# Optimization experiments

Measured on AMD Instinct MI355X. Metric: run time of the kernel, lower is better.

## Reference

```python
import jax, jax.numpy as jnp
import numpy as np

NEG_INF = -1e30  # stands in for -math.inf in masked_fill; -inf itself also works in fp32


def setup_inputs() -> dict:
    key = jax.random.key(0)
    k1, k2, k3, k4, k5 = jax.random.split(key, 5)
    B, T, S, H = 32, 512, 1024, 1024
    query = jax.random.normal(k1, (B, T, H), dtype=jnp.float32)
    encoder_outputs = jax.random.normal(k2, (S, B, H), dtype=jnp.float32)  # seq-first, as in torch RNN outputs
    src_lengths = jax.random.randint(k3, (B,), 1, S + 1, dtype=jnp.int32)
    W_in = jax.random.normal(k4, (H, H), dtype=jnp.float32) / np.sqrt(H)
    W_out = jax.random.normal(k5, (H, 2 * H), dtype=jnp.float32) / np.sqrt(2 * H)
    b_out = jnp.zeros((H,), dtype=jnp.float32)
    return {"query": query, "encoder_outputs": encoder_outputs, "src_lengths": src_lengths,
            "W_in": W_in, "W_out": W_out, "b_out": b_out}


def reference(query, encoder_outputs, src_lengths, W_in, W_out, b_out):
    # query: [B,T,H]; encoder_outputs: [S,B,H] (seq-first)
    # NOTE: the original module computes a length mask but never applies it;
    # instead it fills positions where the raw score is exactly 0 with -inf.
    z = jnp.einsum('bth,ih->bti', query, W_in)                 # linear_in (no bias)
    scores = jnp.einsum('bti,sbi->bts', z, encoder_outputs)    # bmm -> [B,T,S]
    scores = jnp.where(scores == 0, jnp.float32(-jnp.inf), scores)
    p = jax.nn.softmax(scores, axis=2)                         # [B,T,S]
    c = jnp.einsum('bts,sbh->bth', p, encoder_outputs)         # context [B,T,H]
    cat = jnp.concatenate([c, query], axis=2)                  # [B,T,2H]
    attn_h_t = jnp.tanh(jnp.einsum('btk,hk->bth', cat, W_out) + b_out)
    return attn_h_t
```

## Files before the change

kernel.cpp:

```cpp
#include <hip/hip_runtime.h>
#include <math.h>


__device__ inline unsigned short f2bf(float x) {
    unsigned int u = __float_as_uint(x);
    u += 0x7fffu + ((u >> 16) & 1u);
    return (unsigned short)(u >> 16);
}
__device__ inline float bf2f(unsigned short h) {
    return __uint_as_float(((unsigned int)h) << 16);
}
__device__ inline unsigned short f2h(float x) {
    _Float16 h = (_Float16)x;
    return *(unsigned short*)&h;
}

typedef __attribute__((ext_vector_type(8))) short    short8;
typedef __attribute__((ext_vector_type(8))) _Float16 half8;
typedef __attribute__((ext_vector_type(4))) float    f32x4;

__device__ inline void gld_lds16(const void* g, void* l) {
    __builtin_amdgcn_global_load_lds(
        (const __attribute__((address_space(1))) unsigned int*)g,
        (__attribute__((address_space(3))) unsigned int*)l, 16, 0, 0);
}

__device__ inline short8 frag_ld(const short* Ls, int rowbase, int ks8, int lane) {
    const int r = lane & 15, q = lane >> 4;
    return *(const short8*)&Ls[(rowbase + r) * 64 + (((ks8 + q) ^ (r & 7)) << 3)];
}
__device__ inline half8 frag_ld_h(const short* Ls, int rowbase, int ks8, int lane) {
    const int r = lane & 15, q = lane >> 4;
    return *(const half8*)&Ls[(rowbase + r) * 64 + (((ks8 + q) ^ (r & 7)) << 3)];
}

__device__ inline void stage_tile(const unsigned short* g, long ld, short* lds,
                                  int rw, int lr, int gran) {
#pragma unroll
    for (int seg = 0; seg < 4; ++seg) {
        const int row = rw + seg * 8 + lr;
        gld_lds16(g + (long)row * ld + (gran << 3), lds + (rw + seg * 8) * 64);
    }
}

template<int OUT_MODE>
__global__ __launch_bounds__(256, 2)
void gemm_x3(const unsigned short* __restrict__ Ahg, const unsigned short* __restrict__ Alg,
             const unsigned short* __restrict__ Bhg, const unsigned short* __restrict__ Blg,
             float* __restrict__ Of, unsigned short* __restrict__ Oh,
             unsigned short* __restrict__ Ol,
             int K, long lda, long ldb, long ldc, long sA, long sB, long sC)
{
    __shared__ short Ah[128 * 64], Al[128 * 64], Bh[128 * 64], Bl[128 * 64];

    const int tid  = threadIdx.x;
    const int wave = tid >> 6, lane = tid & 63;
    const int wm = (wave & 1) << 6, wn = (wave >> 1) << 6;
    const long m0 = (long)blockIdx.y * 128, n0 = (long)blockIdx.x * 128;
    const int bz = blockIdx.z;

    const unsigned short* Ah0 = Ahg + (long)bz * sA + m0 * lda;
    const unsigned short* Al0 = Alg + (long)bz * sA + m0 * lda;
    const unsigned short* Bh0 = Bhg + (long)bz * sB + n0 * ldb;
    const unsigned short* Bl0 = Blg + (long)bz * sB + n0 * ldb;

    f32x4 acc[4][4];
#pragma unroll
    for (int i = 0; i < 4; ++i)
#pragma unroll
        for (int j = 0; j < 4; ++j) acc[i][j] = (f32x4){0.f, 0.f, 0.f, 0.f};

    const int lr   = lane >> 3;
    const int gran = (lane & 7) ^ lr;
    const int rw   = wave * 32;

    for (int k0 = 0; k0 < K; k0 += 64) {
        __syncthreads();
        stage_tile(Ah0 + k0, lda, Ah, rw, lr, gran);
        stage_tile(Al0 + k0, lda, Al, rw, lr, gran);
        stage_tile(Bh0 + k0, ldb, Bh, rw, lr, gran);
        stage_tile(Bl0 + k0, ldb, Bl, rw, lr, gran);
        __syncthreads();
#pragma unroll
        for (int ks = 0; ks < 2; ++ks) {
            short8 ah[4], al[4], bh[4], bl[4];
#pragma unroll
            for (int i = 0; i < 4; ++i) ah[i] = frag_ld(Ah, wm + i * 16, ks * 4, lane);
#pragma unroll
            for (int j = 0; j < 4; ++j) bh[j] = frag_ld(Bh, wn + j * 16, ks * 4, lane);
#pragma unroll
            for (int i = 0; i < 4; ++i)
#pragma unroll
                for (int j = 0; j < 4; ++j)
                    acc[i][j] = __builtin_amdgcn_mfma_f32_16x16x32_bf16(ah[i], bh[j], acc[i][j], 0, 0, 0);
#pragma unroll
            for (int j = 0; j < 4; ++j) bl[j] = frag_ld(Bl, wn + j * 16, ks * 4, lane);
#pragma unroll
            for (int i = 0; i < 4; ++i)
#pragma unroll
                for (int j = 0; j < 4; ++j)
                    acc[i][j] = __builtin_amdgcn_mfma_f32_16x16x32_bf16(ah[i], bl[j], acc[i][j], 0, 0, 0);
#pragma unroll
            for (int i = 0; i < 4; ++i) al[i] = frag_ld(Al, wm + i * 16, ks * 4, lane);
#pragma unroll
            for (int i = 0; i < 4; ++i)
#pragma unroll
                for (int j = 0; j < 4; ++j)
                    acc[i][j] = __builtin_amdgcn_mfma_f32_16x16x32_bf16(al[i], bh[j], acc[i][j], 0, 0, 0);
        }
    }

    const int q = lane >> 4, r = lane & 15;
#pragma unroll
    for (int i = 0; i < 4; ++i)
#pragma unroll
        for (int rr = 0; rr < 4; ++rr) {
            const long grow = m0 + wm + i * 16 + q * 4 + rr;
#pragma unroll
            for (int j = 0; j < 4; ++j) {
                const long gcol = n0 + wn + j * 16 + r;
                const float v = acc[i][j][rr];
                const long off = (long)bz * sC + grow * ldc + gcol;
                if constexpr (OUT_MODE == 1) {
                    unsigned short h = f2bf(v);
                    Oh[off] = h;
                    Ol[off] = f2bf(v - bf2f(h));
                } else {
                    Of[off] = v;
                }
            }
        }
}

template<int NCHUNK, int OUT_MODE>
__global__ __launch_bounds__(256, 2)
void gemm_f16(const unsigned short* __restrict__ A0, const unsigned short* __restrict__ A1,
              const unsigned short* __restrict__ B0, const unsigned short* __restrict__ B1,
              float* __restrict__ Of, unsigned short* __restrict__ Oh,
              const float* __restrict__ bias,
              int chunkK, long lda, long ldb, long ldc, long sA, long sB, long sC)
{
    __shared__ short As[128 * 64];
    __shared__ short Bs[128 * 64];

    const int tid  = threadIdx.x;
    const int wave = tid >> 6, lane = tid & 63;
    const int wm = (wave & 1) << 6, wn = (wave >> 1) << 6;
    const long m0 = (long)blockIdx.y * 128, n0 = (long)blockIdx.x * 128;
    const int bz = blockIdx.z;

    const unsigned short* Ap[2] = {A0, A1};
    const unsigned short* Bp[2] = {B0, B1};

    f32x4 acc[4][4];
#pragma unroll
    for (int i = 0; i < 4; ++i)
#pragma unroll
        for (int j = 0; j < 4; ++j) acc[i][j] = (f32x4){0.f, 0.f, 0.f, 0.f};

    const int lr   = lane >> 3;
    const int gran = (lane & 7) ^ lr;
    const int rw   = wave * 32;

#pragma unroll
    for (int c = 0; c < NCHUNK; ++c) {
        const unsigned short* Ac = Ap[c] + (long)bz * sA + m0 * lda;
        const unsigned short* Bc = Bp[c] + (long)bz * sB + n0 * ldb;
        for (int k0 = 0; k0 < chunkK; k0 += 64) {
            __syncthreads();
            stage_tile(Ac + k0, lda, As, rw, lr, gran);
            stage_tile(Bc + k0, ldb, Bs, rw, lr, gran);
            __syncthreads();
#pragma unroll
            for (int ks = 0; ks < 2; ++ks) {
                half8 af[4], bfv[4];
#pragma unroll
                for (int i = 0; i < 4; ++i) af[i]  = frag_ld_h(As, wm + i * 16, ks * 4, lane);
#pragma unroll
                for (int j = 0; j < 4; ++j) bfv[j] = frag_ld_h(Bs, wn + j * 16, ks * 4, lane);
#pragma unroll
                for (int i = 0; i < 4; ++i)
#pragma unroll
                    for (int j = 0; j < 4; ++j)
                        acc[i][j] = __builtin_amdgcn_mfma_f32_16x16x32_f16(af[i], bfv[j], acc[i][j], 0, 0, 0);
            }
        }
    }

    const int q = lane >> 4, r = lane & 15;
#pragma unroll
    for (int i = 0; i < 4; ++i)
#pragma unroll
        for (int rr = 0; rr < 4; ++rr) {
            const long grow = m0 + wm + i * 16 + q * 4 + rr;
#pragma unroll
            for (int j = 0; j < 4; ++j) {
                const long gcol = n0 + wn + j * 16 + r;
                const float v = acc[i][j][rr];
                const long off = (long)bz * sC + grow * ldc + gcol;
                if constexpr (OUT_MODE == 0) {
                    Oh[off] = f2h(v);
                } else {
                    Of[off] = tanhf(v + bias[gcol]);
                }
            }
        }
}

template<bool HAS_LO>
__global__ __launch_bounds__(256)
void split_f32_bf16(const float* __restrict__ x, unsigned short* __restrict__ hi,
                    unsigned short* __restrict__ lo, int n4)
{
    const int i = blockIdx.x * 256 + threadIdx.x;
    if (i >= n4) return;
    const float4 v = ((const float4*)x)[i];
    ushort4 h;
    h.x = f2bf(v.x); h.y = f2bf(v.y); h.z = f2bf(v.z); h.w = f2bf(v.w);
    ((ushort4*)hi)[i] = h;
    if constexpr (HAS_LO) {
        ushort4 l;
        l.x = f2bf(v.x - bf2f(h.x)); l.y = f2bf(v.y - bf2f(h.y));
        l.z = f2bf(v.z - bf2f(h.z)); l.w = f2bf(v.w - bf2f(h.w));
        ((ushort4*)lo)[i] = l;
    }
}

__global__ __launch_bounds__(256)
void conv_f32_f16(const float* __restrict__ x, unsigned short* __restrict__ o, int n4)
{
    const int i = blockIdx.x * 256 + threadIdx.x;
    if (i >= n4) return;
    const float4 v = ((const float4*)x)[i];
    ushort4 h;
    h.x = f2h(v.x); h.y = f2h(v.y); h.z = f2h(v.z); h.w = f2h(v.w);
    ((ushort4*)o)[i] = h;
}

__global__ __launch_bounds__(256)
void transpose_enc_f16(const float* __restrict__ E, unsigned short* __restrict__ ET)
{
    __shared__ unsigned short L[64][72];
    const int s0 = blockIdx.x * 64, h0 = blockIdx.y * 64, b = blockIdx.z;
    const int tid = threadIdx.x;
#pragma unroll
    for (int io = 0; io < 2; ++io) {
        const int g = io * 256 + tid;
        const int rs = g >> 3, c8 = (g & 7) * 8;
        const float* src = E + ((long)(s0 + rs) * 32 + b) * 1024 + h0 + c8;
        const float4 v0 = *(const float4*)(src);
        const float4 v1 = *(const float4*)(src + 4);
        L[rs][c8 + 0] = f2h(v0.x); L[rs][c8 + 1] = f2h(v0.y);
        L[rs][c8 + 2] = f2h(v0.z); L[rs][c8 + 3] = f2h(v0.w);
        L[rs][c8 + 4] = f2h(v1.x); L[rs][c8 + 5] = f2h(v1.y);
        L[rs][c8 + 6] = f2h(v1.z); L[rs][c8 + 7] = f2h(v1.w);
    }
    __syncthreads();
#pragma unroll
    for (int io = 0; io < 2; ++io) {
        const int g = io * 256 + tid;
        const int rh = g >> 3, c8 = (g & 7) * 8;
        unsigned short t[8];
#pragma unroll
        for (int j = 0; j < 8; ++j) t[j] = L[c8 + j][rh];
        unsigned short* dst = ET + ((long)b * 1024 + h0 + rh) * 1024 + s0 + c8;
        *(ushort4*)(dst)     = *(const ushort4*)&t[0];
        *(ushort4*)(dst + 4) = *(const ushort4*)&t[4];
    }
}

__global__ __launch_bounds__(256)
void softmax_p_f16(const float* __restrict__ P, unsigned short* __restrict__ Pb)
{
    const int row  = blockIdx.x * 4 + (threadIdx.x >> 6);
    const int lane = threadIdx.x & 63;
    const float* p = P + (long)row * 1024 + lane * 4;
    unsigned short* pb = Pb + (long)row * 1024 + lane * 4;

    float4 v[4];
    float mx = -INFINITY;
#pragma unroll
    for (int i = 0; i < 4; ++i) {
        v[i] = *(const float4*)(p + i * 256);
        v[i].x = (v[i].x == 0.f) ? -INFINITY : v[i].x;
        v[i].y = (v[i].y == 0.f) ? -INFINITY : v[i].y;
        v[i].z = (v[i].z == 0.f) ? -INFINITY : v[i].z;
        v[i].w = (v[i].w == 0.f) ? -INFINITY : v[i].w;
        mx = fmaxf(mx, fmaxf(fmaxf(v[i].x, v[i].y), fmaxf(v[i].z, v[i].w)));
    }
#pragma unroll
    for (int o = 32; o > 0; o >>= 1) mx = fmaxf(mx, __shfl_xor(mx, o, 64));

    float sum = 0.f;
#pragma unroll
    for (int i = 0; i < 4; ++i) {
        v[i].x = __expf(v[i].x - mx); v[i].y = __expf(v[i].y - mx);
        v[i].z = __expf(v[i].z - mx); v[i].w = __expf(v[i].w - mx);
        sum += v[i].x + v[i].y + v[i].z + v[i].w;
    }
#pragma unroll
    for (int o = 32; o > 0; o >>= 1) sum += __shfl_xor(sum, o, 64);

    const float inv = 1.f / sum;
#pragma unroll
    for (int i = 0; i < 4; ++i) {
        ushort4 u;
        u.x = f2h(v[i].x * inv); u.y = f2h(v[i].y * inv);
        u.z = f2h(v[i].z * inv); u.w = f2h(v[i].w * inv);
        *(ushort4*)(pb + i * 256) = u;
    }
}

#define BM 128
#define BN 128
#define BKT 16

template<bool BT, bool DO_TANH, bool CAT_A>
__global__ __launch_bounds__(256)
void sgemm(const float* __restrict__ A, const float* __restrict__ A2,
           const float* __restrict__ Bmat, const float* __restrict__ bias,
           float* __restrict__ C,
           int M, int N, int K, int Ksplit,
           int lda, int ldb, int ldc,
           long sA, long sB, long sC)
{
    __shared__ float Asb[BKT][BM];
    __shared__ float Bsb[BKT][BN];

    const int bz = blockIdx.z;
    const float* Ab = A + (long)bz * sA;
    const float* Bb = Bmat + (long)bz * sB;
    float* Cb = C + (long)bz * sC;

    const int tid = threadIdx.x;
    const int m0 = blockIdx.y * BM;
    const int n0 = blockIdx.x * BN;
    const int tx = tid & 15;
    const int ty = tid >> 4;

    float acc[8][8];
#pragma unroll
    for (int i = 0; i < 8; ++i)
#pragma unroll
        for (int j = 0; j < 8; ++j) acc[i][j] = 0.f;

    for (int kk = 0; kk < K; kk += BKT) {
        const float* Asrc = Ab;
        int acol = kk;
        if constexpr (CAT_A) {
            if (kk >= Ksplit) { Asrc = A2; acol = kk - Ksplit; }
        }
#pragma unroll
        for (int i = 0; i < 2; ++i) {
            int f = i * 256 + tid;
            int row = f >> 2;
            int k4 = (f & 3) << 2;
            float4 v = *(const float4*)(Asrc + (long)(m0 + row) * lda + acol + k4);
            Asb[k4 + 0][row] = v.x; Asb[k4 + 1][row] = v.y;
            Asb[k4 + 2][row] = v.z; Asb[k4 + 3][row] = v.w;
        }
        if constexpr (BT) {
#pragma unroll
            for (int i = 0; i < 2; ++i) {
                int f = i * 256 + tid;
                int row = f >> 2;
                int k4 = (f & 3) << 2;
                float4 v = *(const float4*)(Bb + (long)(n0 + row) * ldb + kk + k4);
                Bsb[k4 + 0][row] = v.x; Bsb[k4 + 1][row] = v.y;
                Bsb[k4 + 2][row] = v.z; Bsb[k4 + 3][row] = v.w;
            }
        } else {
#pragma unroll
            for (int i = 0; i < 2; ++i) {
                int f = i * 256 + tid;
                int kr = f >> 5;
                int n4 = (f & 31) << 2;
                float4 v = *(const float4*)(Bb + (long)(kk + kr) * ldb + n0 + n4);
                *(float4*)&Bsb[kr][n4] = v;
            }
        }
        __syncthreads();
#pragma unroll
        for (int k = 0; k < BKT; ++k) {
            float a[8], bv[8];
            *(float4*)&a[0]  = *(const float4*)&Asb[k][ty * 4];
            *(float4*)&a[4]  = *(const float4*)&Asb[k][ty * 4 + 64];
            *(float4*)&bv[0] = *(const float4*)&Bsb[k][tx * 4];
            *(float4*)&bv[4] = *(const float4*)&Bsb[k][tx * 4 + 64];
#pragma unroll
            for (int i = 0; i < 8; ++i)
#pragma unroll
                for (int j = 0; j < 8; ++j)
                    acc[i][j] = fmaf(a[i], bv[j], acc[i][j]);
        }
        __syncthreads();
    }
#pragma unroll
    for (int i = 0; i < 8; ++i) {
        int rrow = m0 + ty * 4 + (i & 3) + ((i >> 2) << 6);
        float* crow = Cb + (long)rrow * ldc;
#pragma unroll
        for (int jj = 0; jj < 2; ++jj) {
            int c0 = n0 + tx * 4 + jj * 64;
            float4 v;
            v.x = acc[i][jj * 4 + 0]; v.y = acc[i][jj * 4 + 1];
            v.z = acc[i][jj * 4 + 2]; v.w = acc[i][jj * 4 + 3];
            if constexpr (DO_TANH) {
                v.x = tanhf(v.x + bias[c0 + 0]); v.y = tanhf(v.y + bias[c0 + 1]);
                v.z = tanhf(v.z + bias[c0 + 2]); v.w = tanhf(v.w + bias[c0 + 3]);
            }
            *(float4*)(crow + c0) = v;
        }
    }
}

__global__ __launch_bounds__(256)
void softmax_rows(float* __restrict__ P)
{
    const int row = blockIdx.x * 4 + (threadIdx.x >> 6);
    const int lane = threadIdx.x & 63;
    float* p = P + (long)row * 1024 + lane * 4;
    float4 v[4];
    float mx = -INFINITY;
#pragma unroll
    for (int i = 0; i < 4; ++i) {
        v[i] = *(const float4*)(p + i * 256);
        v[i].x = (v[i].x == 0.f) ? -INFINITY : v[i].x;
        v[i].y = (v[i].y == 0.f) ? -INFINITY : v[i].y;
        v[i].z = (v[i].z == 0.f) ? -INFINITY : v[i].z;
        v[i].w = (v[i].w == 0.f) ? -INFINITY : v[i].w;
        mx = fmaxf(mx, fmaxf(fmaxf(v[i].x, v[i].y), fmaxf(v[i].z, v[i].w)));
    }
#pragma unroll
    for (int o = 32; o > 0; o >>= 1) mx = fmaxf(mx, __shfl_xor(mx, o, 64));
    float sum = 0.f;
#pragma unroll
    for (int i = 0; i < 4; ++i) {
        v[i].x = __expf(v[i].x - mx); v[i].y = __expf(v[i].y - mx);
        v[i].z = __expf(v[i].z - mx); v[i].w = __expf(v[i].w - mx);
        sum += v[i].x + v[i].y + v[i].z + v[i].w;
    }
#pragma unroll
    for (int o = 32; o > 0; o >>= 1) sum += __shfl_xor(sum, o, 64);
    const float inv = 1.f / sum;
#pragma unroll
    for (int i = 0; i < 4; ++i) {
        v[i].x *= inv; v[i].y *= inv; v[i].z *= inv; v[i].w *= inv;
        *(float4*)(p + i * 256) = v[i];
    }
}

extern "C" void kernel_launch(void* const* d_in, const int* in_sizes, int n_in,
                              void* d_out, int out_size, void* d_ws, size_t ws_size,
                              hipStream_t stream)
{
    (void)in_sizes; (void)n_in; (void)out_size;
    const int Bv = 32, T = 512, S = 1024, H = 1024;

    const float* q     = (const float*)d_in[0];
    const float* enc   = (const float*)d_in[1];
    const float* W_in  = (const float*)d_in[3];
    const float* W_out = (const float*)d_in[4];
    const float* b_out = (const float*)d_in[5];
    float* out = (float*)d_out;

    const size_t need = 264ull << 20;
    if (ws_size >= need) {
        char* w = (char*)d_ws;
        unsigned short* q_hi  = (unsigned short*)(w);
        unsigned short* q_lo  = (unsigned short*)(w + (32ull << 20));
        unsigned short* z_hi  = (unsigned short*)(w + (64ull << 20));
        unsigned short* z_lo  = (unsigned short*)(w + (96ull << 20));
        unsigned short* e_hi  = (unsigned short*)(w + (128ull << 20));
        unsigned short* e_lo  = (unsigned short*)(w + (192ull << 20));
        unsigned short* Wi_hi = (unsigned short*)(w + (256ull << 20));
        unsigned short* Wi_lo = (unsigned short*)(w + (258ull << 20));
        unsigned short* Wo16  = (unsigned short*)(w + (260ull << 20));

        unsigned short* Pb    = q_lo;
        unsigned short* q16   = z_lo;
        unsigned short* eT    = e_lo;
        unsigned short* C16   = z_hi;

        split_f32_bf16<true ><<<16384, 256, 0, stream>>>(q, q_hi, q_lo, 4194304);
        split_f32_bf16<true ><<<1024,  256, 0, stream>>>(W_in, Wi_hi, Wi_lo, 262144);
        conv_f32_f16<<<2048, 256, 0, stream>>>(W_out, Wo16, 524288);
        split_f32_bf16<true ><<<32768, 256, 0, stream>>>(enc, e_hi, e_lo, 8388608);

        gemm_x3<1><<<dim3(8, 128, 1), 256, 0, stream>>>(
            q_hi, q_lo, Wi_hi, Wi_lo,
            nullptr, z_hi, z_lo,
            1024, 1024, 1024, 1024, 0, 0, 0);

        gemm_x3<2><<<dim3(8, 4, 32), 256, 0, stream>>>(
            z_hi, z_lo, e_hi, e_lo,
            (float*)d_out, nullptr, nullptr,
            1024, 1024, (long)Bv * H, 1024,
            (long)T * H, (long)H, (long)T * S);

        softmax_p_f16<<<(Bv * T) / 4, 256, 0, stream>>>((const float*)d_out, Pb);

        conv_f32_f16<<<16384, 256, 0, stream>>>(q, q16, 4194304);

        transpose_enc_f16<<<dim3(16, 16, 32), 256, 0, stream>>>(enc, eT);

        gemm_f16<1, 0><<<dim3(8, 4, 32), 256, 0, stream>>>(
            Pb, nullptr, eT, nullptr,
            nullptr, C16, nullptr,
            1024, 1024, 1024, 1024,
            (long)T * S, (long)H * S, (long)T * H);

        gemm_f16<2, 3><<<dim3(8, 128, 1), 256, 0, stream>>>(
            C16, q16, Wo16, Wo16 + 1024,
            (float*)d_out, nullptr, b_out,
            1024, 1024, 2048, 1024, 0, 0, 0);
    } else {
        float* Z = (float*)d_ws;
        float* P = Z + (size_t)Bv * T * H;
        dim3 blk(256);
        sgemm<true, false, false><<<dim3(H / BN, (Bv * T) / BM, 1), blk, 0, stream>>>(
            q, nullptr, W_in, nullptr, Z,
            Bv * T, H, H, 0, H, H, H, 0, 0, 0);
        sgemm<true, false, false><<<dim3(S / BN, T / BM, Bv), blk, 0, stream>>>(
            Z, nullptr, enc, nullptr, P,
            T, S, H, 0, H, Bv * H, S, (long)T * H, H, (long)T * S);
        softmax_rows<<<(Bv * T) / 4, blk, 0, stream>>>(P);
        sgemm<false, false, false><<<dim3(H / BN, T / BM, Bv), blk, 0, stream>>>(
            P, nullptr, enc, nullptr, Z,
            T, H, S, 0, S, Bv * H, H, (long)T * S, H, (long)T * H);
        sgemm<true, true, true><<<dim3(H / BN, (Bv * T) / BM, 1), blk, 0, stream>>>(
            Z, q, W_out, b_out, out,
            Bv * T, H, 2 * H, H, H, 2 * H, H, 0, 0, 0);
    }
}
```

Before: 727.4 us.

## Unify GEMMs into triple-buffered 256x128 prefetch-pipelined MFMA kernel

Replaces the separate split-bf16 GEMM and f16 GEMM kernels with one templated kernel, gemm8p. It uses 512 threads and 256x128 tiles. Operands stream through a three-slot LDS ring via global_load_lds, prefetched two K-steps ahead with partial vmcnt waits, so global loads overlap MFMA work. The three-product split-precision sum is rewritten as a 3-chunk concatenated K loop, and MFMA phases are wrapped in s_setprio. The larger tile and ring buffer raise LDS use to about 147KB, which limits occupancy to one block per CU.

```diff
diff --git a/kernel.cpp b/kernel.cpp
--- a/kernel.cpp
+++ b/kernel.cpp
@@ -25,97 +25,155 @@
         (__attribute__((address_space(3))) unsigned int*)l, 16, 0, 0);
 }
 
+#define BAR() do { asm volatile("" ::: "memory"); \
+                   __builtin_amdgcn_s_barrier();  \
+                   asm volatile("" ::: "memory"); } while (0)
+#define VM6() asm volatile("s_waitcnt vmcnt(6)" ::: "memory")
+#define VM0() asm volatile("s_waitcnt vmcnt(0)" ::: "memory")
+
 __device__ inline short8 frag_ld(const short* Ls, int rowbase, int ks8, int lane) {
     const int r = lane & 15, q = lane >> 4;
     return *(const short8*)&Ls[(rowbase + r) * 64 + (((ks8 + q) ^ (r & 7)) << 3)];
 }
-__device__ inline half8 frag_ld_h(const short* Ls, int rowbase, int ks8, int lane) {
-    const int r = lane & 15, q = lane >> 4;
-    return *(const half8*)&Ls[(rowbase + r) * 64 + (((ks8 + q) ^ (r & 7)) << 3)];
-}
-
-__device__ inline void stage_tile(const unsigned short* g, long ld, short* lds,
-                                  int rw, int lr, int gran) {
-#pragma unroll
-    for (int seg = 0; seg < 4; ++seg) {
-        const int row = rw + seg * 8 + lr;
-        gld_lds16(g + (long)row * ld + (gran << 3), lds + (rw + seg * 8) * 64);
-    }
-}
-
-template<int OUT_MODE>
-__global__ __launch_bounds__(256, 2)
-void gemm_x3(const unsigned short* __restrict__ Ahg, const unsigned short* __restrict__ Alg,
-             const unsigned short* __restrict__ Bhg, const unsigned short* __restrict__ Blg,
-             float* __restrict__ Of, unsigned short* __restrict__ Oh,
-             unsigned short* __restrict__ Ol,
-             int K, long lda, long ldb, long ldc, long sA, long sB, long sC)
-{
-    __shared__ short Ah[128 * 64], Al[128 * 64], Bh[128 * 64], Bl[128 * 64];
+
+template<int DT>
+__device__ inline f32x4 mfma16(short8 a, short8 b, f32x4 c) {
+    if constexpr (DT == 0)
+        return __builtin_amdgcn_mfma_f32_16x16x32_bf16(a, b, c, 0, 0, 0);
+    else
+        return __builtin_amdgcn_mfma_f32_16x16x32_f16(
+            __builtin_bit_cast(half8, a), __builtin_bit_cast(half8, b), c, 0, 0, 0);
+}
+
+__device__ inline void stage1(const unsigned short* gk, long ld, short* slot,
+                              int rowbase , int lane) {
+    const int row = rowbase + (lane >> 3);
+    const int g   = (lane & 7) ^ (row & 7);
+    gld_lds16(gk + (long)row * ld + (g << 3), slot + rowbase * 64);
+}
+
+template<int DT, int OUT_MODE>
+__global__ __launch_bounds__(512, 2)
+void gemm8p(const unsigned short* __restrict__ A0, const unsigned short* __restrict__ A1,
+            const unsigned short* __restrict__ A2,
+            const unsigned short* __restrict__ B0, const unsigned short* __restrict__ B1,
+            const unsigned short* __restrict__ B2,
+            float* __restrict__ Of, unsigned short* __restrict__ Oh,
+            unsigned short* __restrict__ Ol, const float* __restrict__ bias,
+            int NT, long lda, long ldb, long ldc, long sA, long sB, long sC)
+{
+    __shared__ short LA[3 * 256 * 64];
+    __shared__ short LB[3 * 128 * 64];
 
     const int tid  = threadIdx.x;
-    const int wave = tid >> 6, lane = tid & 63;
-    const int wm = (wave & 1) << 6, wn = (wave >> 1) << 6;
-    const long m0 = (long)blockIdx.y * 128, n0 = (long)blockIdx.x * 128;
+    const int wid  = tid >> 6, lane = tid & 63;
+    const int wm   = (wid & 3) << 6;
+    const int wn   = (wid >> 2) << 6;
+    const int rb8  = wid << 3;
+    const long m0 = (long)blockIdx.y * 256, n0 = (long)blockIdx.x * 128;
     const int bz = blockIdx.z;
 
-    const unsigned short* Ah0 = Ahg + (long)bz * sA + m0 * lda;
-    const unsigned short* Al0 = Alg + (long)bz * sA + m0 * lda;
-    const unsigned short* Bh0 = Bhg + (long)bz * sB + n0 * ldb;
-    const unsigned short* Bl0 = Blg + (long)bz * sB + n0 * ldb;
-
     f32x4 acc[4][4];
 #pragma unroll
     for (int i = 0; i < 4; ++i)
 #pragma unroll
         for (int j = 0; j < 4; ++j) acc[i][j] = (f32x4){0.f, 0.f, 0.f, 0.f};
 
-    const int lr   = lane >> 3;
-    const int gran = (lane & 7) ^ lr;
-    const int rw   = wave * 32;
-
-    for (int k0 = 0; k0 < K; k0 += 64) {
-        __syncthreads();
-        stage_tile(Ah0 + k0, lda, Ah, rw, lr, gran);
-        stage_tile(Al0 + k0, lda, Al, rw, lr, gran);
-        stage_tile(Bh0 + k0, ldb, Bh, rw, lr, gran);
-        stage_tile(Bl0 + k0, ldb, Bl, rw, lr, gran);
-        __syncthreads();
-#pragma unroll
-        for (int ks = 0; ks < 2; ++ks) {
-            short8 ah[4], al[4], bh[4], bl[4];
-#pragma unroll
-            for (int i = 0; i < 4; ++i) ah[i] = frag_ld(Ah, wm + i * 16, ks * 4, lane);
-#pragma unroll
-            for (int j = 0; j < 4; ++j) bh[j] = frag_ld(Bh, wn + j * 16, ks * 4, lane);
+    {
+        const unsigned short* Ab = A0 + (long)bz * sA + m0 * lda;
+        const unsigned short* Bb = B0 + (long)bz * sB + n0 * ldb;
+#pragma unroll
+        for (int pt = 0; pt < 2; ++pt) {
+            const unsigned short* Ag = Ab + pt * 64;
+            const unsigned short* Bg = Bb + pt * 64;
+            short* As = LA + pt * 16384;
+            short* Bs = LB + pt * 8192;
+            stage1(Ag, lda, As, 0   + rb8, lane);
+            stage1(Ag, lda, As, 64  + rb8, lane);
+            stage1(Ag, lda, As, 128 + rb8, lane);
+            stage1(Ag, lda, As, 192 + rb8, lane);
+            stage1(Bg, ldb, Bs, 0   + rb8, lane);
+            stage1(Bg, ldb, Bs, 64  + rb8, lane);
+        }
+        VM6();
+        BAR();
+    }
+
+    for (int t = 0; t < NT; ++t) {
+        const int s = t % 3;
+        const short* As = LA + s * 16384;
+        const short* Bs = LB + s * 8192;
+
+        const int t2 = t + 2;
+        const bool st = t2 < NT;
+        const unsigned short* A2g = nullptr;
+        const unsigned short* B2g = nullptr;
+        short* As2 = nullptr;
+        short* Bs2 = nullptr;
+        if (st) {
+            const int c2 = t2 >> 4;
+            const long kk2 = (long)(t2 & 15) << 6;
+            const unsigned short* Ac = (c2 == 0) ? A0 : ((c2 == 1) ? A1 : A2);
+            const unsigned short* Bc = (c2 == 0) ? B0 : ((c2 == 1) ? B1 : B2);
+            A2g = Ac + (long)bz * sA + m0 * lda + kk2;
+            B2g = Bc + (long)bz * sB + n0 * ldb + kk2;
+            const int s2 = t2 % 3;
+            As2 = LA + s2 * 16384;
+            Bs2 = LB + s2 * 8192;
+        }
+
+        {
+            short8 a[4], b[4];
+#pragma unroll
+            for (int i = 0; i < 4; ++i) a[i] = frag_ld(As, wm + i * 16, 0, lane);
+#pragma unroll
+            for (int j = 0; j < 4; ++j) b[j] = frag_ld(Bs, wn + j * 16, 0, lane);
+            if (st) {
+                stage1(A2g, lda, As2, 0   + rb8, lane);
+                stage1(A2g, lda, As2, 64  + rb8, lane);
+                stage1(A2g, lda, As2, 128 + rb8, lane);
+            }
+            BAR();
+            __builtin_amdgcn_s_setprio(1);
 #pragma unroll
             for (int i = 0; i < 4; ++i)
 #pragma unroll
                 for (int j = 0; j < 4; ++j)
-                    acc[i][j] = __builtin_amdgcn_mfma_f32_16x16x32_bf16(ah[i], bh[j], acc[i][j], 0, 0, 0);
-#pragma unroll
-            for (int j = 0; j < 4; ++j) bl[j] = frag_ld(Bl, wn + j * 16, ks * 4, lane);
+                    acc[i][j] = mfma16<DT>(a[i], b[j], acc[i][j]);
+            __builtin_amdgcn_s_setprio(0);
+            BAR();
+        }
+
+        {
+            short8 a[4], b[4];
+#pragma unroll
+            for (int i = 0; i < 4; ++i) a[i] = frag_ld(As, wm + i * 16, 4, lane);
+#pragma unroll
+            for (int j = 0; j < 4; ++j) b[j] = frag_ld(Bs, wn + j * 16, 4, lane);
+            if (st) {
+                stage1(A2g, lda, As2, 192 + rb8, lane);
+                stage1(B2g, ldb, Bs2, 0   + rb8, lane);
+                stage1(B2g, ldb, Bs2, 64  + rb8, lane);
+            }
+            if (st) VM6(); else VM0();
+            BAR();
+            __builtin_amdgcn_s_setprio(1);
 #pragma unroll
             for (int i = 0; i < 4; ++i)
 #pragma unroll
                 for (int j = 0; j < 4; ++j)
-                    acc[i][j] = __builtin_amdgcn_mfma_f32_16x16x32_bf16(ah[i], bl[j], acc[i][j], 0, 0, 0);
-#pragma unroll
-            for (int i = 0; i < 4; ++i) al[i] = frag_ld(Al, wm + i * 16, ks * 4, lane);
-#pragma unroll
-            for (int i = 0; i < 4; ++i)
-#pragma unroll
-                for (int j = 0; j < 4; ++j)
-                    acc[i][j] = __builtin_amdgcn_mfma_f32_16x16x32_bf16(al[i], bh[j], acc[i][j], 0, 0, 0);
-        }
-    }
-
-    const int q = lane >> 4, r = lane & 15;
+                    acc[i][j] = mfma16<DT>(a[i], b[j], acc[i][j]);
+            __builtin_amdgcn_s_setprio(0);
+            BAR();
+        }
+    }
+
+    const int qq = lane >> 4, r = lane & 15;
 #pragma unroll
     for (int i = 0; i < 4; ++i)
 #pragma unroll
         for (int rr = 0; rr < 4; ++rr) {
-            const long grow = m0 + wm + i * 16 + q * 4 + rr;
+            const long grow = m0 + wm + i * 16 + qq * 4 + rr;
 #pragma unroll
             for (int j = 0; j < 4; ++j) {
                 const long gcol = n0 + wn + j * 16 + r;
@@ -125,80 +183,9 @@
                     unsigned short h = f2bf(v);
                     Oh[off] = h;
                     Ol[off] = f2bf(v - bf2f(h));
-                } else {
+                } else if constexpr (OUT_MODE == 2) {
                     Of[off] = v;
-                }
-            }
-        }
-}
-
-template<int NCHUNK, int OUT_MODE>
-__global__ __launch_bounds__(256, 2)
-void gemm_f16(const unsigned short* __restrict__ A0, const unsigned short* __restrict__ A1,
-              const unsigned short* __restrict__ B0, const unsigned short* __restrict__ B1,
-              float* __restrict__ Of, unsigned short* __restrict__ Oh,
-              const float* __restrict__ bias,
-              int chunkK, long lda, long ldb, long ldc, long sA, long sB, long sC)
-{
-    __shared__ short As[128 * 64];
-    __shared__ short Bs[128 * 64];
-
-    const int tid  = threadIdx.x;
-    const int wave = tid >> 6, lane = tid & 63;
-    const int wm = (wave & 1) << 6, wn = (wave >> 1) << 6;
-    const long m0 = (long)blockIdx.y * 128, n0 = (long)blockIdx.x * 128;
-    const int bz = blockIdx.z;
-
-    const unsigned short* Ap[2] = {A0, A1};
-    const unsigned short* Bp[2] = {B0, B1};
-
-    f32x4 acc[4][4];
-#pragma unroll
-    for (int i = 0; i < 4; ++i)
-#pragma unroll
-        for (int j = 0; j < 4; ++j) acc[i][j] = (f32x4){0.f, 0.f, 0.f, 0.f};
-
-    const int lr   = lane >> 3;
-    const int gran = (lane & 7) ^ lr;
-    const int rw   = wave * 32;
-
-#pragma unroll
-    for (int c = 0; c < NCHUNK; ++c) {
-        const unsigned short* Ac = Ap[c] + (long)bz * sA + m0 * lda;
-        const unsigned short* Bc = Bp[c] + (long)bz * sB + n0 * ldb;
-        for (int k0 = 0; k0 < chunkK; k0 += 64) {
-            __syncthreads();
-            stage_tile(Ac + k0, lda, As, rw, lr, gran);
-            stage_tile(Bc + k0, ldb, Bs, rw, lr, gran);
-            __syncthreads();
-#pragma unroll
-            for (int ks = 0; ks < 2; ++ks) {
-                half8 af[4], bfv[4];
-#pragma unroll
-                for (int i = 0; i < 4; ++i) af[i]  = frag_ld_h(As, wm + i * 16, ks * 4, lane);
-#pragma unroll
-                for (int j = 0; j < 4; ++j) bfv[j] = frag_ld_h(Bs, wn + j * 16, ks * 4, lane);
-#pragma unroll
-                for (int i = 0; i < 4; ++i)
-#pragma unroll
-                    for (int j = 0; j < 4; ++j)
-                        acc[i][j] = __builtin_amdgcn_mfma_f32_16x16x32_f16(af[i], bfv[j], acc[i][j], 0, 0, 0);
-            }
-        }
-    }
-
-    const int q = lane >> 4, r = lane & 15;
-#pragma unroll
-    for (int i = 0; i < 4; ++i)
-#pragma unroll
-        for (int rr = 0; rr < 4; ++rr) {
-            const long grow = m0 + wm + i * 16 + q * 4 + rr;
-#pragma unroll
-            for (int j = 0; j < 4; ++j) {
-                const long gcol = n0 + wn + j * 16 + r;
-                const float v = acc[i][j][rr];
-                const long off = (long)bz * sC + grow * ldc + gcol;
-                if constexpr (OUT_MODE == 0) {
+                } else if constexpr (OUT_MODE == 0) {
                     Oh[off] = f2h(v);
                 } else {
                     Of[off] = tanhf(v + bias[gcol]);
@@ -487,16 +474,15 @@
         conv_f32_f16<<<2048, 256, 0, stream>>>(W_out, Wo16, 524288);
         split_f32_bf16<true ><<<32768, 256, 0, stream>>>(enc, e_hi, e_lo, 8388608);
 
-        gemm_x3<1><<<dim3(8, 128, 1), 256, 0, stream>>>(
-            q_hi, q_lo, Wi_hi, Wi_lo,
-            nullptr, z_hi, z_lo,
-            1024, 1024, 1024, 1024, 0, 0, 0);
-
-        gemm_x3<2><<<dim3(8, 4, 32), 256, 0, stream>>>(
-            z_hi, z_lo, e_hi, e_lo,
-            (float*)d_out, nullptr, nullptr,
-            1024, 1024, (long)Bv * H, 1024,
-            (long)T * H, (long)H, (long)T * S);
+        gemm8p<0, 1><<<dim3(8, 64, 1), 512, 0, stream>>>(
+            q_hi, q_lo, q_hi, Wi_hi, Wi_hi, Wi_lo,
+            nullptr, z_hi, z_lo, nullptr,
+            48, 1024, 1024, 1024, 0, 0, 0);
+
+        gemm8p<0, 2><<<dim3(8, 2, 32), 512, 0, stream>>>(
+            z_hi, z_lo, z_hi, e_hi, e_hi, e_lo,
+            (float*)d_out, nullptr, nullptr, nullptr,
+            48, 1024, (long)Bv * H, 1024, (long)T * H, (long)H, (long)T * S);
 
         softmax_p_f16<<<(Bv * T) / 4, 256, 0, stream>>>((const float*)d_out, Pb);
 
@@ -504,16 +490,15 @@
 
         transpose_enc_f16<<<dim3(16, 16, 32), 256, 0, stream>>>(enc, eT);
 
-        gemm_f16<1, 0><<<dim3(8, 4, 32), 256, 0, stream>>>(
-            Pb, nullptr, eT, nullptr,
-            nullptr, C16, nullptr,
-            1024, 1024, 1024, 1024,
-            (long)T * S, (long)H * S, (long)T * H);
-
-        gemm_f16<2, 3><<<dim3(8, 128, 1), 256, 0, stream>>>(
-            C16, q16, Wo16, Wo16 + 1024,
-            (float*)d_out, nullptr, b_out,
-            1024, 1024, 2048, 1024, 0, 0, 0);
+        gemm8p<1, 0><<<dim3(8, 2, 32), 512, 0, stream>>>(
+            Pb, nullptr, nullptr, eT, nullptr, nullptr,
+            nullptr, C16, nullptr, nullptr,
+            16, 1024, 1024, 1024, (long)T * S, (long)H * S, (long)T * H);
+
+        gemm8p<1, 3><<<dim3(8, 64, 1), 512, 0, stream>>>(
+            C16, q16, nullptr, Wo16, Wo16 + 1024, nullptr,
+            (float*)d_out, nullptr, nullptr, b_out,
+            32, 1024, 2048, 1024, 0, 0, 0);
     } else {
         float* Z = (float*)d_ws;
         float* P = Z + (size_t)Bv * T * H;
```

Measured after the change: 833.0 us. 14.5% more time.

## Fuse input conversion passes and add XCD-aware block swizzle for flat GEMMs

Applied to the files above, without the earlier changes.

When the workspace is large enough, the query split also writes the fp16 copy, and the encoder split also writes the fp16 transposed copy. This removes the separate re-reads of q and enc that happened later. The two weight-prep kernels are merged into one launch, and the two non-batched GEMMs remap block indices so that each XCD works on a contiguous range of tiles, which should improve L2 reuse. The fused path needs extra workspace (360MB), and if that is not available it falls back to the old aliased buffers.

```diff
diff --git a/kernel.cpp b/kernel.cpp
--- a/kernel.cpp
+++ b/kernel.cpp
@@ -43,7 +43,17 @@
     }
 }
 
-template<int OUT_MODE>
+__device__ inline void xcd_swz(int& bx, int& by) {
+    const int gx = gridDim.x;
+    const int nwg = gx * gridDim.y;
+    const int lin = by * gx + bx;
+    const int cpx = nwg >> 3;
+    const int swz = (lin & 7) * cpx + (lin >> 3);
+    bx = swz % gx;
+    by = swz / gx;
+}
+
+template<int OUT_MODE, bool SWZ>
 __global__ __launch_bounds__(256, 2)
 void gemm_x3(const unsigned short* __restrict__ Ahg, const unsigned short* __restrict__ Alg,
              const unsigned short* __restrict__ Bhg, const unsigned short* __restrict__ Blg,
@@ -56,7 +66,9 @@
     const int tid  = threadIdx.x;
     const int wave = tid >> 6, lane = tid & 63;
     const int wm = (wave & 1) << 6, wn = (wave >> 1) << 6;
-    const long m0 = (long)blockIdx.y * 128, n0 = (long)blockIdx.x * 128;
+    int bxi = blockIdx.x, byi = blockIdx.y;
+    if constexpr (SWZ) xcd_swz(bxi, byi);
+    const long m0 = (long)byi * 128, n0 = (long)bxi * 128;
     const int bz = blockIdx.z;
 
     const unsigned short* Ah0 = Ahg + (long)bz * sA + m0 * lda;
@@ -132,7 +144,7 @@
         }
 }
 
-template<int NCHUNK, int OUT_MODE>
+template<int NCHUNK, int OUT_MODE, bool SWZ>
 __global__ __launch_bounds__(256, 2)
 void gemm_f16(const unsigned short* __restrict__ A0, const unsigned short* __restrict__ A1,
               const unsigned short* __restrict__ B0, const unsigned short* __restrict__ B1,
@@ -146,7 +158,9 @@
     const int tid  = threadIdx.x;
     const int wave = tid >> 6, lane = tid & 63;
     const int wm = (wave & 1) << 6, wn = (wave >> 1) << 6;
-    const long m0 = (long)blockIdx.y * 128, n0 = (long)blockIdx.x * 128;
+    int bxi = blockIdx.x, byi = blockIdx.y;
+    if constexpr (SWZ) xcd_swz(bxi, byi);
+    const long m0 = (long)byi * 128, n0 = (long)bxi * 128;
     const int bz = blockIdx.z;
 
     const unsigned short* Ap[2] = {A0, A1};
@@ -207,23 +221,41 @@
         }
 }
 
-template<bool HAS_LO>
-__global__ __launch_bounds__(256)
-void split_f32_bf16(const float* __restrict__ x, unsigned short* __restrict__ hi,
-                    unsigned short* __restrict__ lo, int n4)
+template<bool Q16>
+__global__ __launch_bounds__(256)
+void split_q_k(const float* __restrict__ x, unsigned short* __restrict__ hi,
+               unsigned short* __restrict__ lo, unsigned short* __restrict__ h16,
+               int n4)
 {
     const int i = blockIdx.x * 256 + threadIdx.x;
     if (i >= n4) return;
     const float4 v = ((const float4*)x)[i];
-    ushort4 h;
+    ushort4 h, l;
     h.x = f2bf(v.x); h.y = f2bf(v.y); h.z = f2bf(v.z); h.w = f2bf(v.w);
+    l.x = f2bf(v.x - bf2f(h.x)); l.y = f2bf(v.y - bf2f(h.y));
+    l.z = f2bf(v.z - bf2f(h.z)); l.w = f2bf(v.w - bf2f(h.w));
     ((ushort4*)hi)[i] = h;
-    if constexpr (HAS_LO) {
-        ushort4 l;
-        l.x = f2bf(v.x - bf2f(h.x)); l.y = f2bf(v.y - bf2f(h.y));
-        l.z = f2bf(v.z - bf2f(h.z)); l.w = f2bf(v.w - bf2f(h.w));
-        ((ushort4*)lo)[i] = l;
-    }
+    ((ushort4*)lo)[i] = l;
+    if constexpr (Q16) {
+        ushort4 f;
+        f.x = f2h(v.x); f.y = f2h(v.y); f.z = f2h(v.z); f.w = f2h(v.w);
+        ((ushort4*)h16)[i] = f;
+    }
+}
+
+__global__ __launch_bounds__(256)
+void split_f32_bf16(const float* __restrict__ x, unsigned short* __restrict__ hi,
+                    unsigned short* __restrict__ lo, int n4)
+{
+    const int i = blockIdx.x * 256 + threadIdx.x;
+    if (i >= n4) return;
+    const float4 v = ((const float4*)x)[i];
+    ushort4 h, l;
+    h.x = f2bf(v.x); h.y = f2bf(v.y); h.z = f2bf(v.z); h.w = f2bf(v.w);
+    l.x = f2bf(v.x - bf2f(h.x)); l.y = f2bf(v.y - bf2f(h.y));
+    l.z = f2bf(v.z - bf2f(h.z)); l.w = f2bf(v.w - bf2f(h.w));
+    ((ushort4*)hi)[i] = h;
+    ((ushort4*)lo)[i] = l;
 }
 
 __global__ __launch_bounds__(256)
@@ -235,6 +267,72 @@
     ushort4 h;
     h.x = f2h(v.x); h.y = f2h(v.y); h.z = f2h(v.z); h.w = f2h(v.w);
     ((ushort4*)o)[i] = h;
+}
+
+__global__ __launch_bounds__(256)
+void prep_w_k(const float* __restrict__ Wi, unsigned short* __restrict__ Wih,
+              unsigned short* __restrict__ Wil,
+              const float* __restrict__ Wo, unsigned short* __restrict__ Wo16)
+{
+    const int i = blockIdx.x * 256 + threadIdx.x;
+    if (i < 262144) {
+        const float4 v = ((const float4*)Wi)[i];
+        ushort4 h, l;
+        h.x = f2bf(v.x); h.y = f2bf(v.y); h.z = f2bf(v.z); h.w = f2bf(v.w);
+        l.x = f2bf(v.x - bf2f(h.x)); l.y = f2bf(v.y - bf2f(h.y));
+        l.z = f2bf(v.z - bf2f(h.z)); l.w = f2bf(v.w - bf2f(h.w));
+        ((ushort4*)Wih)[i] = h;
+        ((ushort4*)Wil)[i] = l;
+    } else {
+        const int j = i - 262144;
+        if (j < 524288) {
+            const float4 v = ((const float4*)Wo)[j];
+            ushort4 h;
+            h.x = f2h(v.x); h.y = f2h(v.y); h.z = f2h(v.z); h.w = f2h(v.w);
+            ((ushort4*)Wo16)[j] = h;
+        }
+    }
+}
+
+__global__ __launch_bounds__(256)
+void split_enc_t(const float* __restrict__ E, unsigned short* __restrict__ Eh,
+                 unsigned short* __restrict__ El, unsigned short* __restrict__ ET)
+{
+    __shared__ unsigned short L[64][72];
+    const int s0 = blockIdx.x * 64, h0 = blockIdx.y * 64, b = blockIdx.z;
+    const int tid = threadIdx.x;
+#pragma unroll
+    for (int io = 0; io < 2; ++io) {
+        const int g = io * 256 + tid;
+        const int rs = g >> 3, c8 = (g & 7) * 8;
+        const long base = ((long)(s0 + rs) * 32 + b) * 1024 + h0 + c8;
+        const float4 v0 = *(const float4*)(E + base);
+        const float4 v1 = *(const float4*)(E + base + 4);
+        const float vv[8] = {v0.x, v0.y, v0.z, v0.w, v1.x, v1.y, v1.z, v1.w};
+        unsigned short hi[8], lo[8];
+#pragma unroll
+        for (int j = 0; j < 8; ++j) {
+            hi[j] = f2bf(vv[j]);
+            lo[j] = f2bf(vv[j] - bf2f(hi[j]));
+            L[rs][c8 + j] = f2h(vv[j]);
+        }
+        *(ushort4*)(Eh + base)     = *(const ushort4*)&hi[0];
+        *(ushort4*)(Eh + base + 4) = *(const ushort4*)&hi[4];
+        *(ushort4*)(El + base)     = *(const ushort4*)&lo[0];
+        *(ushort4*)(El + base + 4) = *(const ushort4*)&lo[4];
+    }
+    __syncthreads();
+#pragma unroll
+    for (int io = 0; io < 2; ++io) {
+        const int g = io * 256 + tid;
+        const int rh = g >> 3, c8 = (g & 7) * 8;
+        unsigned short t[8];
+#pragma unroll
+        for (int j = 0; j < 8; ++j) t[j] = L[c8 + j][rh];
+        unsigned short* dst = ET + ((long)b * 1024 + h0 + rh) * 1024 + s0 + c8;
+        *(ushort4*)(dst)     = *(const ushort4*)&t[0];
+        *(ushort4*)(dst + 4) = *(const ushort4*)&t[4];
+    }
 }
 
 __global__ __launch_bounds__(256)
@@ -466,6 +564,8 @@
 
     const size_t need = 264ull << 20;
     if (ws_size >= need) {
+        const bool big = ws_size >= (360ull << 20);
+
         char* w = (char*)d_ws;
         unsigned short* q_hi  = (unsigned short*)(w);
         unsigned short* q_lo  = (unsigned short*)(w + (32ull << 20));
@@ -476,23 +576,26 @@
         unsigned short* Wi_hi = (unsigned short*)(w + (256ull << 20));
         unsigned short* Wi_lo = (unsigned short*)(w + (258ull << 20));
         unsigned short* Wo16  = (unsigned short*)(w + (260ull << 20));
-
-        unsigned short* Pb    = q_lo;
-        unsigned short* q16   = z_lo;
-        unsigned short* eT    = e_lo;
-        unsigned short* C16   = z_hi;
-
-        split_f32_bf16<true ><<<16384, 256, 0, stream>>>(q, q_hi, q_lo, 4194304);
-        split_f32_bf16<true ><<<1024,  256, 0, stream>>>(W_in, Wi_hi, Wi_lo, 262144);
-        conv_f32_f16<<<2048, 256, 0, stream>>>(W_out, Wo16, 524288);
-        split_f32_bf16<true ><<<32768, 256, 0, stream>>>(enc, e_hi, e_lo, 8388608);
-
-        gemm_x3<1><<<dim3(8, 128, 1), 256, 0, stream>>>(
+        unsigned short* q16b  = (unsigned short*)(w + (264ull << 20));
+        unsigned short* eTb   = (unsigned short*)(w + (296ull << 20));
+
+        unsigned short* Pb  = q_lo;
+        unsigned short* q16 = big ? q16b : z_lo;
+        unsigned short* eT  = big ? eTb  : e_lo;
+        unsigned short* C16 = z_hi;
+
+        if (big) split_q_k<true ><<<16384, 256, 0, stream>>>(q, q_hi, q_lo, q16b, 4194304);
+        else     split_q_k<false><<<16384, 256, 0, stream>>>(q, q_hi, q_lo, nullptr, 4194304);
+        prep_w_k<<<3072, 256, 0, stream>>>(W_in, Wi_hi, Wi_lo, W_out, Wo16);
+        if (big) split_enc_t<<<dim3(16, 16, 32), 256, 0, stream>>>(enc, e_hi, e_lo, eTb);
+        else     split_f32_bf16<<<32768, 256, 0, stream>>>(enc, e_hi, e_lo, 8388608);
+
+        gemm_x3<1, true><<<dim3(8, 128, 1), 256, 0, stream>>>(
             q_hi, q_lo, Wi_hi, Wi_lo,
             nullptr, z_hi, z_lo,
             1024, 1024, 1024, 1024, 0, 0, 0);
 
-        gemm_x3<2><<<dim3(8, 4, 32), 256, 0, stream>>>(
+        gemm_x3<2, false><<<dim3(8, 4, 32), 256, 0, stream>>>(
             z_hi, z_lo, e_hi, e_lo,
             (float*)d_out, nullptr, nullptr,
             1024, 1024, (long)Bv * H, 1024,
@@ -500,17 +603,18 @@
 
         softmax_p_f16<<<(Bv * T) / 4, 256, 0, stream>>>((const float*)d_out, Pb);
 
-        conv_f32_f16<<<16384, 256, 0, stream>>>(q, q16, 4194304);
-
-        transpose_enc_f16<<<dim3(16, 16, 32), 256, 0, stream>>>(enc, eT);
-
-        gemm_f16<1, 0><<<dim3(8, 4, 32), 256, 0, stream>>>(
+        if (!big) {
+            conv_f32_f16<<<16384, 256, 0, stream>>>(q, q16, 4194304);
+            transpose_enc_f16<<<dim3(16, 16, 32), 256, 0, stream>>>(enc, eT);
+        }
+
+        gemm_f16<1, 0, false><<<dim3(8, 4, 32), 256, 0, stream>>>(
             Pb, nullptr, eT, nullptr,
             nullptr, C16, nullptr,
             1024, 1024, 1024, 1024,
             (long)T * S, (long)H * S, (long)T * H);
 
-        gemm_f16<2, 3><<<dim3(8, 128, 1), 256, 0, stream>>>(
+        gemm_f16<2, 3, true><<<dim3(8, 128, 1), 256, 0, stream>>>(
             C16, q16, Wo16, Wo16 + 1024,
             (float*)d_out, nullptr, b_out,
             1024, 1024, 2048, 1024, 0, 0, 0);
```

New measurement: 666.5 us. 8.4% less time.
